# Kernel tuning notes

Measured on AMD Instinct MI355X. Metric: run time of the kernel, lower is better.

The kernel has to match this reference:

```python
import jax, jax.numpy as jnp
import numpy as np

N_USERS = 100000
N_LOCAS = 50000
N = N_USERS + N_LOCAS
D = 128   # embedding_dynamic_size
K = 128   # kg entity dim
S = 128   # static dim
NK = 50000  # kg rows
E = 2048  # number of events
LN_EPS = 1e-5
NORM_EPS = 1e-12


def setup_inputs() -> dict:
    key = jax.random.key(0)
    ks = jax.random.split(key, 24)
    f = jnp.float32
    rin = D + K + 1
    s_rnn = 1.0 / np.sqrt(D)
    s_pred = 1.0 / np.sqrt(2 * S + 2 * D + K)
    inp = {
        'embedding': jax.random.normal(ks[0], (N, D), f),
        'static': jax.random.normal(ks[1], (N, S), f),
        'kg': jax.random.normal(ks[2], (NK, K), f),
        'W_ih_u': jax.random.normal(ks[3], (D, rin), f) * s_rnn,
        'b_ih_u': jax.random.normal(ks[4], (D,), f) * s_rnn,
        'W_hh_u': jax.random.normal(ks[5], (D, D), f) * s_rnn,
        'b_hh_u': jax.random.normal(ks[6], (D,), f) * s_rnn,
        'W_ih_l': jax.random.normal(ks[7], (D, rin), f) * s_rnn,
        'b_ih_l': jax.random.normal(ks[8], (D,), f) * s_rnn,
        'W_hh_l': jax.random.normal(ks[9], (D, D), f) * s_rnn,
        'b_hh_l': jax.random.normal(ks[10], (D,), f) * s_rnn,
        'w_proj': jax.random.normal(ks[11], (D,), f),   # NormalLinear(1, D) weight, std=1/sqrt(1)=1
        'b_proj': jax.random.normal(ks[12], (D,), f),
        'ln_g': jnp.ones((D + K,), f),
        'ln_b': jnp.zeros((D + K,), f),
        'W_pred': jax.random.normal(ks[13], (S + D, 2 * S + 2 * D + K), f) * s_pred,
        'b_pred': jnp.zeros((S + D,), f),
        'delta_u': jax.random.uniform(ks[14], (E,), f),
        'delta_l': jax.random.uniform(ks[15], (E,), f),
        'idx_user': jax.random.randint(ks[16], (E,), 0, N_USERS, jnp.int32),
        'idx_loca': jax.random.randint(ks[17], (E,), 0, N_LOCAS, jnp.int32),
        'idx_prev': jax.random.randint(ks[18], (E,), 0, N_LOCAS, jnp.int32),
        'idx_know': jax.random.randint(ks[19], (E,), 0, NK, jnp.int32),
        'num_users': N_USERS,
    }
    return inp


def reference(embedding, static, kg, W_ih_u, b_ih_u, W_hh_u, b_hh_u,
              W_ih_l, b_ih_l, W_hh_l, b_hh_l, w_proj, b_proj, ln_g, ln_b,
              W_pred, b_pred, delta_u, delta_l,
              idx_user, idx_loca, idx_prev, idx_know, num_users):
    sg = jax.lax.stop_gradient

    def l2n(x):  # F.normalize along the feature dim (row vector)
        return x / jnp.maximum(jnp.linalg.norm(x), NORM_EPS)

    # event index preprocessing (matches idx_loca + num_users etc.)
    xs = (idx_user, idx_loca + num_users, idx_prev + num_users, idx_know,
          delta_u, delta_l)

    def step(carry, ev):
        emb, loss = carry
        iu, il, ip, ik, du, dl = ev
        u = emb[iu]        # [D]
        l = emb[il]        # [D]
        p = emb[ip]        # [D]
        kgr = kg[ik]       # [K]
        # projection: u * (1 + Linear(1->D)(delta_u))
        proj = u * (1.0 + w_proj * du + b_proj)
        # layer_norm over concat([emb_prev, kg_row]) of size D+K
        x = jnp.concatenate([p, kgr])
        mu = x.mean()
        var = jnp.mean((x - mu) ** 2)
        ln = (x - mu) / jnp.sqrt(var + LN_EPS) * ln_g + ln_b
        meta = jnp.concatenate([proj, ln, static[ip], static[iu]])  # [2S+2D+K]
        pred = W_pred @ meta + b_pred                               # [S+D]
        tgt = jnp.concatenate([l, static[il]])
        loss_pred = jnp.mean((pred - sg(tgt)) ** 2)
        # RNNCell updates (tanh), then L2-normalize
        x_u = jnp.concatenate([l, kgr, du[None]])
        new_u = l2n(jnp.tanh(W_ih_u @ x_u + b_ih_u + W_hh_u @ u + b_hh_u))
        x_l = jnp.concatenate([u, kgr, dl[None]])
        new_l = l2n(jnp.tanh(W_ih_l @ x_l + b_ih_l + W_hh_l @ l + b_hh_l))
        loss = loss + loss_pred \
                    + jnp.mean((new_u - sg(u)) ** 2) \
                    + jnp.mean((new_l - sg(l)) ** 2)
        emb = emb.at[iu].set(new_u).at[il].set(new_l)
        return (emb, loss), None

    (emb, loss), _ = jax.lax.scan(
        step, (embedding, jnp.asarray(0.0, embedding.dtype)), xs)
    return emb, loss
```

## Files before the change

### kernel.cpp

```cpp
#include <hip/hip_runtime.h>

#define DEVINL static __device__ __forceinline__

typedef float f32x4 __attribute__((ext_vector_type(4)));

constexpr int NUSER = 100000;
constexpr int D     = 128;
constexpr int METAN = 640;
constexpr int NT    = 256;
constexpr int CH    = 4;
constexpr int KP4   = 160;
constexpr int KR4   = 96;
constexpr int NCPY  = 2048;

struct Params {
  const float *emb_in, *stat, *kg;
  const float *Wihu, *bihu, *Whhu, *bhhu;
  const float *Wihl, *bihl, *Whhl, *bhhl;
  const float *wproj, *bproj, *lng, *lnb, *Wpred, *bpred;
  const float *deltau, *deltal;
  const int *idxu, *idxl, *idxp, *idxk;
  float *emb;
  float *loss_slot;
  float *WpredT;
  float *WrnnT;
  float *brnn;
  float *wcol;
  float *loss_ev;
  int *cnt_u, *cnt_w, *cnt_t;
  int *flag_u, *flag_l;
  int E, N, NLOC, NWORK;
};

DEVINL float loadx(const float* p) {
  return __hip_atomic_load(p, __ATOMIC_RELAXED, __HIP_MEMORY_SCOPE_AGENT);
}
DEVINL void storex(float* p, float v) {
  __hip_atomic_store(p, v, __ATOMIC_RELAXED, __HIP_MEMORY_SCOPE_AGENT);
}
DEVINL int loadcnt(const int* p) {
  return __hip_atomic_load(p, __ATOMIC_RELAXED, __HIP_MEMORY_SCOPE_AGENT);
}
DEVINL void sigadd(int* pp) {
  __hip_atomic_fetch_add(pp, 1, __ATOMIC_RELAXED, __HIP_MEMORY_SCOPE_AGENT);
}
DEVINL float dot4(float4 a, float4 b) { return a.x*b.x + a.y*b.y + a.z*b.z + a.w*b.w; }

DEVINL float4 block_sum4(float4 v, float4* s4) {
  #pragma unroll
  for (int o = 32; o; o >>= 1) {
    v.x += __shfl_xor(v.x, o, 64); v.y += __shfl_xor(v.y, o, 64);
    v.z += __shfl_xor(v.z, o, 64); v.w += __shfl_xor(v.w, o, 64);
  }
  if ((threadIdx.x & 63) == 0) s4[threadIdx.x >> 6] = v;
  __syncthreads();
  float4 r;
  r.x = s4[0].x + s4[1].x + s4[2].x + s4[3].x;
  r.y = s4[0].y + s4[1].y + s4[2].y + s4[3].y;
  r.z = s4[0].z + s4[1].z + s4[2].z + s4[3].z;
  r.w = s4[0].w + s4[1].w + s4[2].w + s4[3].w;
  __syncthreads();
  return r;
}

DEVINL void half_sum4(float4 v, float4* s4, float4* lo, float4* hi) {
  #pragma unroll
  for (int o = 32; o; o >>= 1) {
    v.x += __shfl_xor(v.x, o, 64); v.y += __shfl_xor(v.y, o, 64);
    v.z += __shfl_xor(v.z, o, 64); v.w += __shfl_xor(v.w, o, 64);
  }
  if ((threadIdx.x & 63) == 0) s4[threadIdx.x >> 6] = v;
  __syncthreads();
  lo->x = s4[0].x + s4[1].x; lo->y = s4[0].y + s4[1].y;
  lo->z = s4[0].z + s4[1].z; lo->w = s4[0].w + s4[1].w;
  hi->x = s4[2].x + s4[3].x; hi->y = s4[2].y + s4[3].y;
  hi->z = s4[2].z + s4[3].z; hi->w = s4[2].w + s4[3].w;
  __syncthreads();
}

__global__ void k_init(Params p) {
  int tid = blockIdx.x * NT + threadIdx.x;
  int stride = gridDim.x * NT;
  for (int e = tid; e < p.E; e += stride) {
    p.flag_u[p.idxu[e]] = 1;
    p.flag_l[p.idxl[e]] = 1;
  }
  for (int idx = tid; idx < 256 * KP4; idx += stride) {
    int j = idx / KP4, k4 = idx - j * KP4;
    float4 v = *(const float4*)(p.Wpred + (size_t)j * METAN + k4 * 4);
    ((float4*)p.WpredT)[k4 * 256 + j] = v;
  }
  for (int idx = tid; idx < 256 * KR4; idx += stride) {
    int j = idx / KR4, k4 = idx - j * KR4;
    int i = j & 127;
    const float* Wih = (j < 128) ? p.Wihu : p.Wihl;
    const float* Whh = (j < 128) ? p.Whhu : p.Whhl;
    float4 v; float* vp = (float*)&v;
    #pragma unroll
    for (int e = 0; e < 4; ++e) {
      int k = k4 * 4 + e;
      vp[e] = (k < 256) ? Wih[(size_t)i * 257 + k] : Whh[(size_t)i * 128 + (k - 256)];
    }
    ((float4*)p.WrnnT)[k4 * 256 + j] = v;
  }
  for (int j = tid; j < 256; j += stride) {
    int i = j & 127;
    p.brnn[j] = (j < 128) ? p.bihu[i] + p.bhhu[i] : p.bihl[i] + p.bhhl[i];
    p.wcol[j] = (j < 128) ? p.Wihu[(size_t)i * 257 + 256] : p.Wihl[(size_t)i * 257 + 256];
  }
}

__global__ __launch_bounds__(NT) void k_copy(Params p) {
  size_t gid = (size_t)blockIdx.x * NT + threadIdx.x;
  size_t gs  = (size_t)gridDim.x * NT;
  size_t n4  = (size_t)p.N * 32;
  const f32x4* src = (const f32x4*)p.emb_in;
  f32x4* dst = (f32x4*)p.emb;
  size_t g = gid;
  for (; g + 3 * gs < n4; g += 4 * gs) {
    size_t g0 = g, g1 = g + gs, g2 = g + 2 * gs, g3 = g + 3 * gs;
    int r0 = (int)(g0 >> 5), r1 = (int)(g1 >> 5), r2 = (int)(g2 >> 5), r3 = (int)(g3 >> 5);
    int f0 = (r0 < NUSER) ? p.flag_u[r0] : p.flag_l[r0 - NUSER];
    int f1 = (r1 < NUSER) ? p.flag_u[r1] : p.flag_l[r1 - NUSER];
    int f2 = (r2 < NUSER) ? p.flag_u[r2] : p.flag_l[r2 - NUSER];
    int f3 = (r3 < NUSER) ? p.flag_u[r3] : p.flag_l[r3 - NUSER];
    f32x4 v0 = src[g0], v1 = src[g1], v2 = src[g2], v3 = src[g3];
    if (!f0) dst[g0] = v0;
    if (!f1) dst[g1] = v1;
    if (!f2) dst[g2] = v2;
    if (!f3) dst[g3] = v3;
  }
  for (; g < n4; g += gs) {
    int r = (int)(g >> 5);
    int f = (r < NUSER) ? p.flag_u[r] : p.flag_l[r - NUSER];
    f32x4 v = src[g];
    if (!f) dst[g] = v;
  }
}

__global__ __launch_bounds__(NT, 2) void k_events(Params p) {
  __shared__ __align__(16) float s_meta[CH][METAN];
  __shared__ __align__(16) float s_u[CH][D], s_l[CH][D], s_p[CH][D], s_kg[CH][D], s_sil[CH][D];
  __shared__ float4 s_r4[4];
  __shared__ unsigned long long s_redu[4][CH];
  __shared__ int s_ev[8][CH];
  __shared__ float s_dd[2][CH];

  const int tid = threadIdx.x, w = tid >> 6, lane = tid & 63;

  const int base = blockIdx.x * CH;
  const int nev  = min(CH, p.E - base);
  if (nev <= 0) return;

  int iu_[CH], il_[CH], ip_[CH], ik_[CH];
  float du_[CH], dl_[CH];
  #pragma unroll
  for (int e = 0; e < CH; ++e) {
    int t = base + e; bool v = e < nev;
    iu_[e] = v ? p.idxu[t] : -1;
    il_[e] = v ? p.idxl[t] : -1;
    ip_[e] = v ? p.idxp[t] : -1;
    ik_[e] = v ? p.idxk[t] : 0;
    du_[e] = v ? p.deltau[t] : 0.f;
    dl_[e] = v ? p.deltal[t] : 0.f;
  }

  unsigned long long pk[CH] = {0ull,0ull,0ull,0ull};
  for (int s = tid; s < base; s += NT) {
    int ius = p.idxu[s], ils = p.idxl[s], ips = p.idxp[s];
    #pragma unroll
    for (int e = 0; e < CH; ++e) {
      unsigned long long a  = (ius == iu_[e]);
      unsigned long long wl = (ils == il_[e]);
      unsigned long long b  = (unsigned long long)((ils == il_[e]) + (ips == il_[e]));
      unsigned long long c  = (ils == ip_[e]);
      pk[e] += a | (wl << 16) | (b << 32) | (c << 48);
    }
  }
  #pragma unroll
  for (int o = 32; o; o >>= 1) {
    #pragma unroll
    for (int e = 0; e < CH; ++e) pk[e] += __shfl_xor(pk[e], o, 64);
  }
  if (lane == 0) {
    #pragma unroll
    for (int e = 0; e < CH; ++e) s_redu[w][e] = pk[e];
  }
  __syncthreads();
  #pragma unroll
  for (int e = 0; e < CH; ++e)
    pk[e] = s_redu[0][e] + s_redu[1][e] + s_redu[2][e] + s_redu[3][e];
  __syncthreads();

  int A_[CH], WL_[CH], B_[CH], C_[CH];
  #pragma unroll
  for (int e = 0; e < CH; ++e) {
    int a  = (int)(pk[e] & 0xffff),        wl = (int)((pk[e] >> 16) & 0xffff);
    int b  = (int)((pk[e] >> 32) & 0xffff), c = (int)((pk[e] >> 48) & 0xffff);
    #pragma unroll
    for (int s2 = 0; s2 < CH; ++s2) if (s2 < e) {
      a  += (iu_[s2] == iu_[e]);
      wl += (il_[s2] == il_[e]);
      b  += (il_[s2] == il_[e]) + (ip_[s2] == il_[e]);
      c  += (il_[s2] == ip_[e]);
    }
    A_[e] = a; WL_[e] = wl; B_[e] = b; C_[e] = c;
  }
  bool internal = false;
  #pragma unroll
  for (int t2 = 1; t2 < CH; ++t2) if (t2 < nev) {
    #pragma unroll
    for (int s2 = 0; s2 < t2; ++s2)
      internal |= (iu_[s2] == iu_[t2]) | (il_[s2] == il_[t2]) |
                  (il_[s2] == ip_[t2]) | (ip_[s2] == il_[t2]);
  }

  if (tid == 0) {
    #pragma unroll
    for (int e = 0; e < CH; ++e) {
      s_ev[0][e] = iu_[e]; s_ev[1][e] = il_[e]; s_ev[2][e] = ip_[e];
      s_ev[3][e] = A_[e];  s_ev[4][e] = WL_[e]; s_ev[5][e] = B_[e];
      s_ev[6][e] = C_[e];  s_ev[7][e] = ik_[e];
      s_dd[0][e] = du_[e]; s_dd[1][e] = dl_[e];
    }
  }
  __syncthreads();

  auto PRELOAD = [&](int b0, int b1) {
    int e = w;
    if (e >= b0 && e < b1) {
      int iu = s_ev[0][e], ilr = s_ev[1][e] + NUSER, ipr = s_ev[2][e] + NUSER;
      int A = s_ev[3][e], WL = s_ev[4][e], Ck = s_ev[6][e], ik = s_ev[7][e];
      int h2 = lane >> 5, li = (lane & 31) * 4;
      if (h2 == 0) {
        *(float4*)&s_kg[e][li]         = *(const float4*)(p.kg   + (size_t)ik  * D + li);
        *(float4*)&s_meta[e][512 + li] = *(const float4*)(p.stat + (size_t)iu  * D + li);
      } else {
        *(float4*)&s_meta[e][384 + li] = *(const float4*)(p.stat + (size_t)ipr * D + li);
        *(float4*)&s_sil[e][li]        = *(const float4*)(p.stat + (size_t)ilr * D + li);
      }
      int i0 = lane * 2;
      if (!A) {
        *(float2*)&s_u[e][i0] = *(const float2*)(p.emb_in + (size_t)iu * D + i0);
      }
      if (!WL) {
        *(float2*)&s_l[e][i0] = *(const float2*)(p.emb_in + (size_t)ilr * D + i0);
      }
      if (!Ck) {
        *(float2*)&s_p[e][i0] = *(const float2*)(p.emb_in + (size_t)ipr * D + i0);
      }
    }
  };

  auto SPIN = [&](int b0, int b1) {
    if (w == 0) {
      int e = b0 + lane;
      bool act = lane < (b1 - b0);
      int iu = 0, il = 0, ip = 0, A = 0, Bc = 0, Cc = 0;
      if (act) {
        iu = s_ev[0][e]; il = s_ev[1][e]; ip = s_ev[2][e];
        A = s_ev[3][e]; Bc = s_ev[5][e]; Cc = s_ev[6][e];
      }
      int guard = 0;
      while (true) {
        int x = loadcnt(&p.cnt_u[iu]);
        int y = loadcnt(&p.cnt_t[il]);
        int z = loadcnt(&p.cnt_w[ip]);
        bool ok = (!act) | ((x >= A) & (y >= Bc) & (z >= Cc));
        if (__all(ok)) break;
        if (++guard > (1 << 22)) break;
        __builtin_amdgcn_s_sleep(1);
      }
    }
    __syncthreads();
  };

  auto POSTLOAD = [&](int b0, int b1) {
    int e = w;
    if (e >= b0 && e < b1) {
      int iu = s_ev[0][e], ilr = s_ev[1][e] + NUSER, ipr = s_ev[2][e] + NUSER;
      int A = s_ev[3][e], WL = s_ev[4][e], Ck = s_ev[6][e];
      int i0 = lane * 2;
      if (A) {
        s_u[e][i0]   = loadx(p.emb + (size_t)iu * D + i0);
        s_u[e][i0+1] = loadx(p.emb + (size_t)iu * D + i0 + 1);
      }
      if (WL) {
        s_l[e][i0]   = loadx(p.emb + (size_t)ilr * D + i0);
        s_l[e][i0+1] = loadx(p.emb + (size_t)ilr * D + i0 + 1);
      }
      if (Ck) {
        s_p[e][i0]   = loadx(p.emb + (size_t)ipr * D + i0);
        s_p[e][i0+1] = loadx(p.emb + (size_t)ipr * D + i0 + 1);
      }
    }
  };

  auto PROCESS = [&](int b0, int b1) {
    __syncthreads();

    const bool uc = (tid < 128);
    const float4* xo0 = (const float4*)(uc ? s_l[0] : s_u[0]);
    const float4* xo1 = (const float4*)(uc ? s_l[1] : s_u[1]);
    const float4* xo2 = (const float4*)(uc ? s_l[2] : s_u[2]);
    const float4* xo3 = (const float4*)(uc ? s_l[3] : s_u[3]);
    const float4* xk0 = (const float4*)s_kg[0];
    const float4* xk1 = (const float4*)s_kg[1];
    const float4* xk2 = (const float4*)s_kg[2];
    const float4* xk3 = (const float4*)s_kg[3];
    const float4* xs0 = (const float4*)(uc ? s_u[0] : s_l[0]);
    const float4* xs1 = (const float4*)(uc ? s_u[1] : s_l[1]);
    const float4* xs2 = (const float4*)(uc ? s_u[2] : s_l[2]);
    const float4* xs3 = (const float4*)(uc ? s_u[3] : s_l[3]);
    float ra0 = 0.f, ra1 = 0.f, ra2 = 0.f, ra3 = 0.f;
    const float4* wr = (const float4*)p.WrnnT + tid;
    #pragma unroll 8
    for (int k4 = 0; k4 < 32; ++k4) {
      float4 wv = wr[k4 * 256];
      ra0 += dot4(wv, xo0[k4]); ra1 += dot4(wv, xo1[k4]);
      ra2 += dot4(wv, xo2[k4]); ra3 += dot4(wv, xo3[k4]);
    }
    #pragma unroll 8
    for (int k4 = 32; k4 < 64; ++k4) {
      float4 wv = wr[k4 * 256];
      ra0 += dot4(wv, xk0[k4-32]); ra1 += dot4(wv, xk1[k4-32]);
      ra2 += dot4(wv, xk2[k4-32]); ra3 += dot4(wv, xk3[k4-32]);
    }
    #pragma unroll 8
    for (int k4 = 64; k4 < 96; ++k4) {
      float4 wv = wr[k4 * 256];
      ra0 += dot4(wv, xs0[k4-64]); ra1 += dot4(wv, xs1[k4-64]);
      ra2 += dot4(wv, xs2[k4-64]); ra3 += dot4(wv, xs3[k4-64]);
    }
    float brn = p.brnn[tid], wcv = p.wcol[tid];
    float d0 = uc ? s_dd[0][0] : s_dd[1][0];
    float d1 = uc ? s_dd[0][1] : s_dd[1][1];
    float d2 = uc ? s_dd[0][2] : s_dd[1][2];
    float d3 = uc ? s_dd[0][3] : s_dd[1][3];
    float h0 = tanhf(ra0 + brn + wcv * d0), h1 = tanhf(ra1 + brn + wcv * d1);
    float h2v = tanhf(ra2 + brn + wcv * d2), h3 = tanhf(ra3 + brn + wcv * d3);

    float4 SU, SL;
    half_sum4(make_float4(h0*h0, h1*h1, h2v*h2v, h3*h3), s_r4, &SU, &SL);
    float s0 = uc ? SU.x : SL.x, s1 = uc ? SU.y : SL.y;
    float s2 = uc ? SU.z : SL.z, s3 = uc ? SU.w : SL.w;
    float n0 = h0 / fmaxf(sqrtf(s0), 1e-12f), n1 = h1 / fmaxf(sqrtf(s1), 1e-12f);
    float n2 = h2v / fmaxf(sqrtf(s2), 1e-12f), n3 = h3 / fmaxf(sqrtf(s3), 1e-12f);

    float nv[CH] = {n0, n1, n2, n3};
    #pragma unroll
    for (int e = 0; e < CH; ++e) if (e >= b0 && e < b1) {
      if (tid < 128) storex(p.emb + (size_t)s_ev[0][e] * D + tid, nv[e]);
      else           storex(p.emb + ((size_t)s_ev[1][e] + NUSER) * D + (tid - 128), nv[e]);
    }
    __syncthreads();

    if (tid >= b0 && tid < b1) {
      __builtin_amdgcn_fence(__ATOMIC_RELEASE, "agent");
      sigadd(&p.cnt_u[s_ev[0][tid]]);
      sigadd(&p.cnt_t[s_ev[1][tid]]);
      sigadd(&p.cnt_w[s_ev[1][tid]]);
      sigadd(&p.cnt_t[s_ev[2][tid]]);
    }

    {
      int e = w;
      if (e >= b0 && e < b1) {
        float du = s_dd[0][e];
        float4 xv = (lane < 32) ? *(const float4*)&s_p[e][lane * 4]
                                : *(const float4*)&s_kg[e][(lane - 32) * 4];
        float sm = xv.x + xv.y + xv.z + xv.w;
        #pragma unroll
        for (int o = 32; o; o >>= 1) sm += __shfl_xor(sm, o, 64);
        float mu = sm * (1.f / 256.f);
        float4 d = make_float4(xv.x - mu, xv.y - mu, xv.z - mu, xv.w - mu);
        float vs = d.x*d.x + d.y*d.y + d.z*d.z + d.w*d.w;
        #pragma unroll
        for (int o = 32; o; o >>= 1) vs += __shfl_xor(vs, o, 64);
        float rstd = rsqrtf(vs * (1.f / 256.f) + 1e-5f);
        int idx = lane * 4;
        float4 g  = *(const float4*)&p.lng[idx];
        float4 bb = *(const float4*)&p.lnb[idx];
        *(float4*)&s_meta[e][128 + idx] = make_float4(
          d.x*rstd*g.x + bb.x, d.y*rstd*g.y + bb.y,
          d.z*rstd*g.z + bb.z, d.w*rstd*g.w + bb.w);

        int i0 = lane * 2;
        #pragma unroll
        for (int j = 0; j < 2; ++j) {
          int i = i0 + j;
          s_meta[e][i] = s_u[e][i] * (1.f + p.wproj[i] * du + p.bproj[i]);
        }
      }
    }
    __syncthreads();

    const float4* m40 = (const float4*)&s_meta[0][0];
    const float4* m41 = (const float4*)&s_meta[1][0];
    const float4* m42 = (const float4*)&s_meta[2][0];
    const float4* m43 = (const float4*)&s_meta[3][0];
    float pa0 = 0.f, pa1 = 0.f, pa2 = 0.f, pa3 = 0.f;
    const float4* wp = (const float4*)p.WpredT + tid;
    #pragma unroll 8
    for (int k4 = 0; k4 < KP4; ++k4) {
      float4 wv = wp[k4 * 256];
      pa0 += dot4(wv, m40[k4]); pa1 += dot4(wv, m41[k4]);
      pa2 += dot4(wv, m42[k4]); pa3 += dot4(wv, m43[k4]);
    }
    float bp = p.bpred[tid];
    float4 ep2;
    {
      float tg0 = uc ? s_l[0][tid] : s_sil[0][tid - 128];
      float tg1 = uc ? s_l[1][tid] : s_sil[1][tid - 128];
      float tg2 = uc ? s_l[2][tid] : s_sil[2][tid - 128];
      float tg3 = uc ? s_l[3][tid] : s_sil[3][tid - 128];
      float e0 = pa0 + bp - tg0, e1 = pa1 + bp - tg1;
      float e2 = pa2 + bp - tg2, e3 = pa3 + bp - tg3;
      ep2 = make_float4(e0*e0, e1*e1, e2*e2, e3*e3);
    }
    float4 LP = block_sum4(ep2, s_r4);

    float o0 = uc ? s_u[0][tid] : s_l[0][tid - 128];
    float o1 = uc ? s_u[1][tid] : s_l[1][tid - 128];
    float o2 = uc ? s_u[2][tid] : s_l[2][tid - 128];
    float o3 = uc ? s_u[3][tid] : s_l[3][tid - 128];
    float q0 = n0 - o0, q1 = n1 - o1, q2 = n2 - o2, q3 = n3 - o3;
    float4 LE = block_sum4(make_float4(q0*q0, q1*q1, q2*q2, q3*q3), s_r4);

    if (tid >= b0 && tid < b1) {
      float lp = (tid == 0) ? LP.x : (tid == 1) ? LP.y : (tid == 2) ? LP.z : LP.w;
      float le = (tid == 0) ? LE.x : (tid == 1) ? LE.y : (tid == 2) ? LE.z : LE.w;
      p.loss_ev[base + tid] = lp * (1.f / 256.f) + le * (1.f / 128.f);
    }
  };

  if (!internal) {
    PRELOAD(0, nev);
    SPIN(0, nev);
    POSTLOAD(0, nev);
    PROCESS(0, nev);
  } else {
    for (int e = 0; e < nev; ++e) {
      PRELOAD(e, e + 1);
      SPIN(e, e + 1);
      POSTLOAD(e, e + 1);
      PROCESS(e, e + 1);
    }
  }
}

__global__ void k_fin(Params p) {
  __shared__ float4 s_r4[4];
  float v = 0.f;
  for (int i = threadIdx.x; i < p.E; i += NT) v += p.loss_ev[i];
  float4 r = block_sum4(make_float4(v, 0.f, 0.f, 0.f), s_r4);
  if (threadIdx.x == 0) p.loss_slot[0] = r.x;
}

extern "C" void kernel_launch(void* const* d_in, const int* in_sizes, int n_in,
                              void* d_out, int out_size, void* d_ws, size_t ws_size,
                              hipStream_t stream) {
  Params p;
  p.emb_in = (const float*)d_in[0];
  p.stat   = (const float*)d_in[1];
  p.kg     = (const float*)d_in[2];
  p.Wihu = (const float*)d_in[3];   p.bihu = (const float*)d_in[4];
  p.Whhu = (const float*)d_in[5];   p.bhhu = (const float*)d_in[6];
  p.Wihl = (const float*)d_in[7];   p.bihl = (const float*)d_in[8];
  p.Whhl = (const float*)d_in[9];   p.bhhl = (const float*)d_in[10];
  p.wproj = (const float*)d_in[11]; p.bproj = (const float*)d_in[12];
  p.lng  = (const float*)d_in[13];  p.lnb  = (const float*)d_in[14];
  p.Wpred = (const float*)d_in[15]; p.bpred = (const float*)d_in[16];
  p.deltau = (const float*)d_in[17];
  p.deltal = (const float*)d_in[18];
  p.idxu = (const int*)d_in[19];
  p.idxl = (const int*)d_in[20];
  p.idxp = (const int*)d_in[21];
  p.idxk = (const int*)d_in[22];

  p.E    = in_sizes[17];
  p.N    = in_sizes[0] / D;
  p.NLOC = p.N - NUSER;
  p.NWORK = (p.E + CH - 1) / CH;

  p.emb       = (float*)d_out;
  p.loss_slot = (float*)d_out + (size_t)p.N * D;

  char* ws = (char*)d_ws;
  size_t off = 0;
  auto take = [&](size_t bytes) {
    void* r = ws + off;
    off += (bytes + 255) & ~(size_t)255;
    return r;
  };
  p.WpredT  = (float*)take((size_t)KP4 * 256 * 16);
  p.WrnnT   = (float*)take((size_t)KR4 * 256 * 16);
  p.brnn    = (float*)take(256 * 4);
  p.wcol    = (float*)take(256 * 4);
  p.loss_ev = (float*)take((size_t)p.E * 4);
  size_t z0 = off;
  p.cnt_u   = (int*)take((size_t)NUSER * 4);
  p.cnt_w   = (int*)take((size_t)p.NLOC * 4);
  p.cnt_t   = (int*)take((size_t)p.NLOC * 4);
  p.flag_u  = (int*)take((size_t)NUSER * 4);
  p.flag_l  = (int*)take((size_t)p.NLOC * 4);
  size_t zbytes = off - z0;

  hipMemsetAsync(ws + z0, 0, zbytes, stream);
  hipLaunchKernelGGL(k_init,   dim3(512),    dim3(NT), 0, stream, p);
  hipLaunchKernelGGL(k_copy,   dim3(NCPY),   dim3(NT), 0, stream, p);
  hipLaunchKernelGGL(k_events, dim3(p.NWORK),dim3(NT), 0, stream, p);
  hipLaunchKernelGGL(k_fin,    dim3(1),      dim3(NT), 0, stream, p);
}
```

Measured before the change: 173.8 us.

## Fuse copy into event kernel and split RNN chain from prediction-loss blocks

```diff
diff --git a/kernel.cpp b/kernel.cpp
--- a/kernel.cpp
+++ b/kernel.cpp
@@ -11,7 +11,8 @@
 constexpr int CH    = 4;
 constexpr int KP4   = 160;
 constexpr int KR4   = 96;
-constexpr int NCPY  = 2048;
+constexpr int NCPY  = 1024;
+constexpr int STW   = 640;
 
 struct Params {
   const float *emb_in, *stat, *kg;
@@ -27,8 +28,10 @@
   float *brnn;
   float *wcol;
   float *loss_ev;
+  float *stash;
   int *cnt_u, *cnt_w, *cnt_t;
   int *flag_u, *flag_l;
+  int *done;
   int E, N, NLOC, NWORK;
 };
 
@@ -40,6 +43,9 @@
 }
 DEVINL int loadcnt(const int* p) {
   return __hip_atomic_load(p, __ATOMIC_RELAXED, __HIP_MEMORY_SCOPE_AGENT);
+}
+DEVINL void storei(int* p, int v) {
+  __hip_atomic_store(p, v, __ATOMIC_RELAXED, __HIP_MEMORY_SCOPE_AGENT);
 }
 DEVINL void sigadd(int* pp) {
   __hip_atomic_fetch_add(pp, 1, __ATOMIC_RELAXED, __HIP_MEMORY_SCOPE_AGENT);
@@ -110,35 +116,7 @@
   }
 }
 
-__global__ __launch_bounds__(NT) void k_copy(Params p) {
-  size_t gid = (size_t)blockIdx.x * NT + threadIdx.x;
-  size_t gs  = (size_t)gridDim.x * NT;
-  size_t n4  = (size_t)p.N * 32;
-  const f32x4* src = (const f32x4*)p.emb_in;
-  f32x4* dst = (f32x4*)p.emb;
-  size_t g = gid;
-  for (; g + 3 * gs < n4; g += 4 * gs) {
-    size_t g0 = g, g1 = g + gs, g2 = g + 2 * gs, g3 = g + 3 * gs;
-    int r0 = (int)(g0 >> 5), r1 = (int)(g1 >> 5), r2 = (int)(g2 >> 5), r3 = (int)(g3 >> 5);
-    int f0 = (r0 < NUSER) ? p.flag_u[r0] : p.flag_l[r0 - NUSER];
-    int f1 = (r1 < NUSER) ? p.flag_u[r1] : p.flag_l[r1 - NUSER];
-    int f2 = (r2 < NUSER) ? p.flag_u[r2] : p.flag_l[r2 - NUSER];
-    int f3 = (r3 < NUSER) ? p.flag_u[r3] : p.flag_l[r3 - NUSER];
-    f32x4 v0 = src[g0], v1 = src[g1], v2 = src[g2], v3 = src[g3];
-    if (!f0) dst[g0] = v0;
-    if (!f1) dst[g1] = v1;
-    if (!f2) dst[g2] = v2;
-    if (!f3) dst[g3] = v3;
-  }
-  for (; g < n4; g += gs) {
-    int r = (int)(g >> 5);
-    int f = (r < NUSER) ? p.flag_u[r] : p.flag_l[r - NUSER];
-    f32x4 v = src[g];
-    if (!f) dst[g] = v;
-  }
-}
-
-__global__ __launch_bounds__(NT, 2) void k_events(Params p) {
+__global__ __launch_bounds__(NT, 2) void k_main(Params p) {
   __shared__ __align__(16) float s_meta[CH][METAN];
   __shared__ __align__(16) float s_u[CH][D], s_l[CH][D], s_p[CH][D], s_kg[CH][D], s_sil[CH][D];
   __shared__ float4 s_r4[4];
@@ -147,13 +125,44 @@
   __shared__ float s_dd[2][CH];
 
   const int tid = threadIdx.x, w = tid >> 6, lane = tid & 63;
-
-  const int base = blockIdx.x * CH;
-  const int nev  = min(CH, p.E - base);
+  const int bid = blockIdx.x;
+
+  if (bid >= p.NWORK && bid < p.NWORK + NCPY) {
+    size_t gid = (size_t)(bid - p.NWORK) * NT + tid;
+    size_t gs  = (size_t)NCPY * NT;
+    size_t n4  = (size_t)p.N * 32;
+    const f32x4* src = (const f32x4*)p.emb_in;
+    f32x4* dst = (f32x4*)p.emb;
+    size_t g = gid;
+    for (; g + 3 * gs < n4; g += 4 * gs) {
+      size_t g0 = g, g1 = g + gs, g2 = g + 2 * gs, g3 = g + 3 * gs;
+      int r0 = (int)(g0 >> 5), r1 = (int)(g1 >> 5), r2 = (int)(g2 >> 5), r3 = (int)(g3 >> 5);
+      int f0 = (r0 < NUSER) ? p.flag_u[r0] : p.flag_l[r0 - NUSER];
+      int f1 = (r1 < NUSER) ? p.flag_u[r1] : p.flag_l[r1 - NUSER];
+      int f2 = (r2 < NUSER) ? p.flag_u[r2] : p.flag_l[r2 - NUSER];
+      int f3 = (r3 < NUSER) ? p.flag_u[r3] : p.flag_l[r3 - NUSER];
+      f32x4 v0 = src[g0], v1 = src[g1], v2 = src[g2], v3 = src[g3];
+      if (!f0) dst[g0] = v0;
+      if (!f1) dst[g1] = v1;
+      if (!f2) dst[g2] = v2;
+      if (!f3) dst[g3] = v3;
+    }
+    for (; g < n4; g += gs) {
+      int r = (int)(g >> 5);
+      int f = (r < NUSER) ? p.flag_u[r] : p.flag_l[r - NUSER];
+      f32x4 v = src[g];
+      if (!f) dst[g] = v;
+    }
+    return;
+  }
+
+  const bool is_chain = (bid < p.NWORK);
+  const int c = is_chain ? bid : bid - p.NWORK - NCPY;
+  const int base = c * CH;
+  const int nev = min(CH, p.E - base);
   if (nev <= 0) return;
 
   int iu_[CH], il_[CH], ip_[CH], ik_[CH];
-  float du_[CH], dl_[CH];
   #pragma unroll
   for (int e = 0; e < CH; ++e) {
     int t = base + e; bool v = e < nev;
@@ -161,76 +170,258 @@
     il_[e] = v ? p.idxl[t] : -1;
     ip_[e] = v ? p.idxp[t] : -1;
     ik_[e] = v ? p.idxk[t] : 0;
-    du_[e] = v ? p.deltau[t] : 0.f;
-    dl_[e] = v ? p.deltal[t] : 0.f;
-  }
-
-  unsigned long long pk[CH] = {0ull,0ull,0ull,0ull};
-  for (int s = tid; s < base; s += NT) {
-    int ius = p.idxu[s], ils = p.idxl[s], ips = p.idxp[s];
+  }
+
+  if (is_chain) {
+    float du_[CH], dl_[CH];
     #pragma unroll
     for (int e = 0; e < CH; ++e) {
-      unsigned long long a  = (ius == iu_[e]);
-      unsigned long long wl = (ils == il_[e]);
-      unsigned long long b  = (unsigned long long)((ils == il_[e]) + (ips == il_[e]));
-      unsigned long long c  = (ils == ip_[e]);
-      pk[e] += a | (wl << 16) | (b << 32) | (c << 48);
-    }
-  }
-  #pragma unroll
-  for (int o = 32; o; o >>= 1) {
+      int t = base + e; bool v = e < nev;
+      du_[e] = v ? p.deltau[t] : 0.f;
+      dl_[e] = v ? p.deltal[t] : 0.f;
+    }
+
+    unsigned long long pk[CH] = {0ull,0ull,0ull,0ull};
+    for (int s = tid; s < base; s += NT) {
+      int ius = p.idxu[s], ils = p.idxl[s], ips = p.idxp[s];
+      #pragma unroll
+      for (int e = 0; e < CH; ++e) {
+        unsigned long long a  = (ius == iu_[e]);
+        unsigned long long wl = (ils == il_[e]);
+        unsigned long long b  = (unsigned long long)((ils == il_[e]) + (ips == il_[e]));
+        unsigned long long cc = (ils == ip_[e]);
+        pk[e] += a | (wl << 16) | (b << 32) | (cc << 48);
+      }
+    }
     #pragma unroll
-    for (int e = 0; e < CH; ++e) pk[e] += __shfl_xor(pk[e], o, 64);
-  }
-  if (lane == 0) {
+    for (int o = 32; o; o >>= 1) {
+      #pragma unroll
+      for (int e = 0; e < CH; ++e) pk[e] += __shfl_xor(pk[e], o, 64);
+    }
+    if (lane == 0) {
+      #pragma unroll
+      for (int e = 0; e < CH; ++e) s_redu[w][e] = pk[e];
+    }
+    __syncthreads();
     #pragma unroll
-    for (int e = 0; e < CH; ++e) s_redu[w][e] = pk[e];
-  }
-  __syncthreads();
-  #pragma unroll
-  for (int e = 0; e < CH; ++e)
-    pk[e] = s_redu[0][e] + s_redu[1][e] + s_redu[2][e] + s_redu[3][e];
-  __syncthreads();
-
-  int A_[CH], WL_[CH], B_[CH], C_[CH];
-  #pragma unroll
-  for (int e = 0; e < CH; ++e) {
-    int a  = (int)(pk[e] & 0xffff),        wl = (int)((pk[e] >> 16) & 0xffff);
-    int b  = (int)((pk[e] >> 32) & 0xffff), c = (int)((pk[e] >> 48) & 0xffff);
-    #pragma unroll
-    for (int s2 = 0; s2 < CH; ++s2) if (s2 < e) {
-      a  += (iu_[s2] == iu_[e]);
-      wl += (il_[s2] == il_[e]);
-      b  += (il_[s2] == il_[e]) + (ip_[s2] == il_[e]);
-      c  += (il_[s2] == ip_[e]);
-    }
-    A_[e] = a; WL_[e] = wl; B_[e] = b; C_[e] = c;
-  }
-  bool internal = false;
-  #pragma unroll
-  for (int t2 = 1; t2 < CH; ++t2) if (t2 < nev) {
-    #pragma unroll
-    for (int s2 = 0; s2 < t2; ++s2)
-      internal |= (iu_[s2] == iu_[t2]) | (il_[s2] == il_[t2]) |
-                  (il_[s2] == ip_[t2]) | (ip_[s2] == il_[t2]);
-  }
-
-  if (tid == 0) {
+    for (int e = 0; e < CH; ++e)
+      pk[e] = s_redu[0][e] + s_redu[1][e] + s_redu[2][e] + s_redu[3][e];
+    __syncthreads();
+
+    int A_[CH], WL_[CH], B_[CH], C_[CH];
     #pragma unroll
     for (int e = 0; e < CH; ++e) {
-      s_ev[0][e] = iu_[e]; s_ev[1][e] = il_[e]; s_ev[2][e] = ip_[e];
-      s_ev[3][e] = A_[e];  s_ev[4][e] = WL_[e]; s_ev[5][e] = B_[e];
-      s_ev[6][e] = C_[e];  s_ev[7][e] = ik_[e];
-      s_dd[0][e] = du_[e]; s_dd[1][e] = dl_[e];
-    }
-  }
-  __syncthreads();
-
-  auto PRELOAD = [&](int b0, int b1) {
-    int e = w;
-    if (e >= b0 && e < b1) {
-      int iu = s_ev[0][e], ilr = s_ev[1][e] + NUSER, ipr = s_ev[2][e] + NUSER;
-      int A = s_ev[3][e], WL = s_ev[4][e], Ck = s_ev[6][e], ik = s_ev[7][e];
+      int a  = (int)(pk[e] & 0xffff),        wl = (int)((pk[e] >> 16) & 0xffff);
+      int b  = (int)((pk[e] >> 32) & 0xffff), cc = (int)((pk[e] >> 48) & 0xffff);
+      #pragma unroll
+      for (int s2 = 0; s2 < CH; ++s2) if (s2 < e) {
+        a  += (iu_[s2] == iu_[e]);
+        wl += (il_[s2] == il_[e]);
+        b  += (il_[s2] == il_[e]) + (ip_[s2] == il_[e]);
+        cc += (il_[s2] == ip_[e]);
+      }
+      A_[e] = a; WL_[e] = wl; B_[e] = b; C_[e] = cc;
+    }
+    bool internal = false;
+    #pragma unroll
+    for (int t2 = 1; t2 < CH; ++t2) if (t2 < nev) {
+      #pragma unroll
+      for (int s2 = 0; s2 < t2; ++s2)
+        internal |= (iu_[s2] == iu_[t2]) | (il_[s2] == il_[t2]) |
+                    (il_[s2] == ip_[t2]) | (ip_[s2] == il_[t2]);
+    }
+
+    if (tid == 0) {
+      #pragma unroll
+      for (int e = 0; e < CH; ++e) {
+        s_ev[0][e] = iu_[e]; s_ev[1][e] = il_[e]; s_ev[2][e] = ip_[e];
+        s_ev[3][e] = A_[e];  s_ev[4][e] = WL_[e]; s_ev[5][e] = B_[e];
+        s_ev[6][e] = C_[e];  s_ev[7][e] = ik_[e];
+        s_dd[0][e] = du_[e]; s_dd[1][e] = dl_[e];
+      }
+    }
+    __syncthreads();
+
+    auto PRELOAD = [&](int b0, int b1) {
+      int e = w;
+      if (e >= b0 && e < b1) {
+        int iu = s_ev[0][e], ilr = s_ev[1][e] + NUSER, ipr = s_ev[2][e] + NUSER;
+        int A = s_ev[3][e], WL = s_ev[4][e], Ck = s_ev[6][e], ik = s_ev[7][e];
+        if (lane < 32) {
+          int li = lane * 4;
+          *(float4*)&s_kg[e][li] = *(const float4*)(p.kg + (size_t)ik * D + li);
+        }
+        int i0 = lane * 2;
+        if (!A)  *(float2*)&s_u[e][i0] = *(const float2*)(p.emb_in + (size_t)iu  * D + i0);
+        if (!WL) *(float2*)&s_l[e][i0] = *(const float2*)(p.emb_in + (size_t)ilr * D + i0);
+        if (!Ck) *(float2*)&s_p[e][i0] = *(const float2*)(p.emb_in + (size_t)ipr * D + i0);
+      }
+    };
+
+    auto SPIN = [&](int b0, int b1) {
+      if (w == 0) {
+        int e = b0 + lane;
+        bool act = lane < (b1 - b0);
+        int iu = 0, il = 0, ip = 0, A = 0, Bc = 0, Cc = 0;
+        if (act) {
+          iu = s_ev[0][e]; il = s_ev[1][e]; ip = s_ev[2][e];
+          A = s_ev[3][e]; Bc = s_ev[5][e]; Cc = s_ev[6][e];
+        }
+        int guard = 0;
+        while (true) {
+          int x = loadcnt(&p.cnt_u[iu]);
+          int y = loadcnt(&p.cnt_t[il]);
+          int z = loadcnt(&p.cnt_w[ip]);
+          bool ok = (!act) | ((x >= A) & (y >= Bc) & (z >= Cc));
+          if (__all(ok)) break;
+          if (++guard > (1 << 22)) break;
+          __builtin_amdgcn_s_sleep(1);
+        }
+      }
+      __syncthreads();
+    };
+
+    auto POSTLOAD = [&](int b0, int b1) {
+      int e = w;
+      if (e >= b0 && e < b1) {
+        int iu = s_ev[0][e], ilr = s_ev[1][e] + NUSER, ipr = s_ev[2][e] + NUSER;
+        int A = s_ev[3][e], WL = s_ev[4][e], Ck = s_ev[6][e];
+        int i0 = lane * 2;
+        if (A) {
+          s_u[e][i0]   = loadx(p.emb + (size_t)iu * D + i0);
+          s_u[e][i0+1] = loadx(p.emb + (size_t)iu * D + i0 + 1);
+        }
+        if (WL) {
+          s_l[e][i0]   = loadx(p.emb + (size_t)ilr * D + i0);
+          s_l[e][i0+1] = loadx(p.emb + (size_t)ilr * D + i0 + 1);
+        }
+        if (Ck) {
+          s_p[e][i0]   = loadx(p.emb + (size_t)ipr * D + i0);
+          s_p[e][i0+1] = loadx(p.emb + (size_t)ipr * D + i0 + 1);
+        }
+      }
+    };
+
+    auto RNNPROC = [&](int b0, int b1) {
+      __syncthreads();
+      const bool uc = (tid < 128);
+      const float4* xo0 = (const float4*)(uc ? s_l[0] : s_u[0]);
+      const float4* xo1 = (const float4*)(uc ? s_l[1] : s_u[1]);
+      const float4* xo2 = (const float4*)(uc ? s_l[2] : s_u[2]);
+      const float4* xo3 = (const float4*)(uc ? s_l[3] : s_u[3]);
+      const float4* xk0 = (const float4*)s_kg[0];
+      const float4* xk1 = (const float4*)s_kg[1];
+      const float4* xk2 = (const float4*)s_kg[2];
+      const float4* xk3 = (const float4*)s_kg[3];
+      const float4* xs0 = (const float4*)(uc ? s_u[0] : s_l[0]);
+      const float4* xs1 = (const float4*)(uc ? s_u[1] : s_l[1]);
+      const float4* xs2 = (const float4*)(uc ? s_u[2] : s_l[2]);
+      const float4* xs3 = (const float4*)(uc ? s_u[3] : s_l[3]);
+      float ra0 = 0.f, ra1 = 0.f, ra2 = 0.f, ra3 = 0.f;
+      const float4* wr = (const float4*)p.WrnnT + tid;
+      #pragma unroll 8
+      for (int k4 = 0; k4 < 32; ++k4) {
+        float4 wv = wr[k4 * 256];
+        ra0 += dot4(wv, xo0[k4]); ra1 += dot4(wv, xo1[k4]);
+        ra2 += dot4(wv, xo2[k4]); ra3 += dot4(wv, xo3[k4]);
+      }
+      #pragma unroll 8
+      for (int k4 = 32; k4 < 64; ++k4) {
+        float4 wv = wr[k4 * 256];
+        ra0 += dot4(wv, xk0[k4-32]); ra1 += dot4(wv, xk1[k4-32]);
+        ra2 += dot4(wv, xk2[k4-32]); ra3 += dot4(wv, xk3[k4-32]);
+      }
+      #pragma unroll 8
+      for (int k4 = 64; k4 < 96; ++k4) {
+        float4 wv = wr[k4 * 256];
+        ra0 += dot4(wv, xs0[k4-64]); ra1 += dot4(wv, xs1[k4-64]);
+        ra2 += dot4(wv, xs2[k4-64]); ra3 += dot4(wv, xs3[k4-64]);
+      }
+      float brn = p.brnn[tid], wcv = p.wcol[tid];
+      float d0 = uc ? s_dd[0][0] : s_dd[1][0];
+      float d1 = uc ? s_dd[0][1] : s_dd[1][1];
+      float d2 = uc ? s_dd[0][2] : s_dd[1][2];
+      float d3 = uc ? s_dd[0][3] : s_dd[1][3];
+      float h0 = tanhf(ra0 + brn + wcv * d0), h1 = tanhf(ra1 + brn + wcv * d1);
+      float h2v = tanhf(ra2 + brn + wcv * d2), h3 = tanhf(ra3 + brn + wcv * d3);
+
+      float4 SU, SL;
+      half_sum4(make_float4(h0*h0, h1*h1, h2v*h2v, h3*h3), s_r4, &SU, &SL);
+      float s0 = uc ? SU.x : SL.x, s1 = uc ? SU.y : SL.y;
+      float s2 = uc ? SU.z : SL.z, s3 = uc ? SU.w : SL.w;
+      float n0 = h0 / fmaxf(sqrtf(s0), 1e-12f), n1 = h1 / fmaxf(sqrtf(s1), 1e-12f);
+      float n2 = h2v / fmaxf(sqrtf(s2), 1e-12f), n3 = h3 / fmaxf(sqrtf(s3), 1e-12f);
+
+      float nv[CH] = {n0, n1, n2, n3};
+      #pragma unroll
+      for (int e = 0; e < CH; ++e) if (e >= b0 && e < b1) {
+        if (tid < 128) storex(p.emb + (size_t)s_ev[0][e] * D + tid, nv[e]);
+        else           storex(p.emb + ((size_t)s_ev[1][e] + NUSER) * D + (tid - 128), nv[e]);
+      }
+      __syncthreads();
+
+      if (tid >= b0 && tid < b1) {
+        __builtin_amdgcn_fence(__ATOMIC_RELEASE, "agent");
+        sigadd(&p.cnt_u[s_ev[0][tid]]);
+        sigadd(&p.cnt_t[s_ev[1][tid]]);
+        sigadd(&p.cnt_w[s_ev[1][tid]]);
+        sigadd(&p.cnt_t[s_ev[2][tid]]);
+      }
+
+      #pragma unroll
+      for (int e = 0; e < CH; ++e) if (e >= b0 && e < b1) {
+        float* st = p.stash + (size_t)(base + e) * STW;
+        if (tid < 128) {
+          storex(st + tid,       s_u[e][tid]);
+          storex(st + 256 + tid, s_p[e][tid]);
+          storex(st + 384 + tid, nv[e]);
+        } else {
+          int i = tid - 128;
+          storex(st + 128 + i, s_l[e][i]);
+          storex(st + 512 + i, nv[e]);
+        }
+      }
+    };
+
+    if (!internal) {
+      PRELOAD(0, nev);
+      SPIN(0, nev);
+      POSTLOAD(0, nev);
+      RNNPROC(0, nev);
+    } else {
+      for (int e = 0; e < nev; ++e) {
+        PRELOAD(e, e + 1);
+        SPIN(e, e + 1);
+        POSTLOAD(e, e + 1);
+        RNNPROC(e, e + 1);
+      }
+    }
+    __syncthreads();
+    if (tid == 0) storei(&p.done[c], 1);
+    return;
+  }
+
+  {
+    if (w == 0) {
+      int guard = 0;
+      while (!loadcnt(&p.done[c])) {
+        if (++guard > (1 << 22)) break;
+        __builtin_amdgcn_s_sleep(1);
+      }
+    }
+    __syncthreads();
+
+    if (w < nev) {
+      int e = w;
+      const float* st = p.stash + (size_t)(base + e) * STW;
+      int iu = iu_[e], ilr = il_[e] + NUSER, ipr = ip_[e] + NUSER, ik = ik_[e];
+      int i0 = lane * 2;
+      s_u[e][i0]   = loadx(st + i0);
+      s_u[e][i0+1] = loadx(st + i0 + 1);
+      s_l[e][i0]   = loadx(st + 128 + i0);
+      s_l[e][i0+1] = loadx(st + 128 + i0 + 1);
+      s_p[e][i0]   = loadx(st + 256 + i0);
+      s_p[e][i0+1] = loadx(st + 256 + i0 + 1);
       int h2 = lane >> 5, li = (lane & 31) * 4;
       if (h2 == 0) {
         *(float4*)&s_kg[e][li]         = *(const float4*)(p.kg   + (size_t)ik  * D + li);
@@ -239,162 +430,40 @@
         *(float4*)&s_meta[e][384 + li] = *(const float4*)(p.stat + (size_t)ipr * D + li);
         *(float4*)&s_sil[e][li]        = *(const float4*)(p.stat + (size_t)ilr * D + li);
       }
+    }
+    __syncthreads();
+
+    if (w < nev) {
+      int e = w;
+      float du = p.deltau[base + e];
+      float4 xv = (lane < 32) ? *(const float4*)&s_p[e][lane * 4]
+                              : *(const float4*)&s_kg[e][(lane - 32) * 4];
+      float sm = xv.x + xv.y + xv.z + xv.w;
+      #pragma unroll
+      for (int o = 32; o; o >>= 1) sm += __shfl_xor(sm, o, 64);
+      float mu = sm * (1.f / 256.f);
+      float4 d = make_float4(xv.x - mu, xv.y - mu, xv.z - mu, xv.w - mu);
+      float vs = d.x*d.x + d.y*d.y + d.z*d.z + d.w*d.w;
+      #pragma unroll
+      for (int o = 32; o; o >>= 1) vs += __shfl_xor(vs, o, 64);
+      float rstd = rsqrtf(vs * (1.f / 256.f) + 1e-5f);
+      int idx2 = lane * 4;
+      float4 g  = *(const float4*)&p.lng[idx2];
+      float4 bb = *(const float4*)&p.lnb[idx2];
+      float4 lnv = make_float4(d.x*rstd*g.x + bb.x, d.y*rstd*g.y + bb.y,
+                               d.z*rstd*g.z + bb.z, d.w*rstd*g.w + bb.w);
+      if (lane < 32) *(float4*)&s_meta[e][128 + idx2] = lnv;
+      else           *(float4*)&s_meta[e][128 + idx2] = lnv;
       int i0 = lane * 2;
-      if (!A) {
-        *(float2*)&s_u[e][i0] = *(const float2*)(p.emb_in + (size_t)iu * D + i0);
-      }
-      if (!WL) {
-        *(float2*)&s_l[e][i0] = *(const float2*)(p.emb_in + (size_t)ilr * D + i0);
-      }
-      if (!Ck) {
-        *(float2*)&s_p[e][i0] = *(const float2*)(p.emb_in + (size_t)ipr * D + i0);
-      }
-    }
-  };
-
-  auto SPIN = [&](int b0, int b1) {
-    if (w == 0) {
-      int e = b0 + lane;
-      bool act = lane < (b1 - b0);
-      int iu = 0, il = 0, ip = 0, A = 0, Bc = 0, Cc = 0;
-      if (act) {
-        iu = s_ev[0][e]; il = s_ev[1][e]; ip = s_ev[2][e];
-        A = s_ev[3][e]; Bc = s_ev[5][e]; Cc = s_ev[6][e];
-      }
-      int guard = 0;
-      while (true) {
-        int x = loadcnt(&p.cnt_u[iu]);
-        int y = loadcnt(&p.cnt_t[il]);
-        int z = loadcnt(&p.cnt_w[ip]);
-        bool ok = (!act) | ((x >= A) & (y >= Bc) & (z >= Cc));
-        if (__all(ok)) break;
-        if (++guard > (1 << 22)) break;
-        __builtin_amdgcn_s_sleep(1);
-      }
-    }
-    __syncthreads();
-  };
-
-  auto POSTLOAD = [&](int b0, int b1) {
-    int e = w;
-    if (e >= b0 && e < b1) {
-      int iu = s_ev[0][e], ilr = s_ev[1][e] + NUSER, ipr = s_ev[2][e] + NUSER;
-      int A = s_ev[3][e], WL = s_ev[4][e], Ck = s_ev[6][e];
-      int i0 = lane * 2;
-      if (A) {
-        s_u[e][i0]   = loadx(p.emb + (size_t)iu * D + i0);
-        s_u[e][i0+1] = loadx(p.emb + (size_t)iu * D + i0 + 1);
-      }
-      if (WL) {
-        s_l[e][i0]   = loadx(p.emb + (size_t)ilr * D + i0);
-        s_l[e][i0+1] = loadx(p.emb + (size_t)ilr * D + i0 + 1);
-      }
-      if (Ck) {
-        s_p[e][i0]   = loadx(p.emb + (size_t)ipr * D + i0);
-        s_p[e][i0+1] = loadx(p.emb + (size_t)ipr * D + i0 + 1);
-      }
-    }
-  };
-
-  auto PROCESS = [&](int b0, int b1) {
+      #pragma unroll
+      for (int j = 0; j < 2; ++j) {
+        int i = i0 + j;
+        s_meta[e][i] = s_u[e][i] * (1.f + p.wproj[i] * du + p.bproj[i]);
+      }
+    }
     __syncthreads();
 
     const bool uc = (tid < 128);
-    const float4* xo0 = (const float4*)(uc ? s_l[0] : s_u[0]);
-    const float4* xo1 = (const float4*)(uc ? s_l[1] : s_u[1]);
-    const float4* xo2 = (const float4*)(uc ? s_l[2] : s_u[2]);
-    const float4* xo3 = (const float4*)(uc ? s_l[3] : s_u[3]);
-    const float4* xk0 = (const float4*)s_kg[0];
-    const float4* xk1 = (const float4*)s_kg[1];
-    const float4* xk2 = (const float4*)s_kg[2];
-    const float4* xk3 = (const float4*)s_kg[3];
-    const float4* xs0 = (const float4*)(uc ? s_u[0] : s_l[0]);
-    const float4* xs1 = (const float4*)(uc ? s_u[1] : s_l[1]);
-    const float4* xs2 = (const float4*)(uc ? s_u[2] : s_l[2]);
-    const float4* xs3 = (const float4*)(uc ? s_u[3] : s_l[3]);
-    float ra0 = 0.f, ra1 = 0.f, ra2 = 0.f, ra3 = 0.f;
-    const float4* wr = (const float4*)p.WrnnT + tid;
-    #pragma unroll 8
-    for (int k4 = 0; k4 < 32; ++k4) {
-      float4 wv = wr[k4 * 256];
-      ra0 += dot4(wv, xo0[k4]); ra1 += dot4(wv, xo1[k4]);
-      ra2 += dot4(wv, xo2[k4]); ra3 += dot4(wv, xo3[k4]);
-    }
-    #pragma unroll 8
-    for (int k4 = 32; k4 < 64; ++k4) {
-      float4 wv = wr[k4 * 256];
-      ra0 += dot4(wv, xk0[k4-32]); ra1 += dot4(wv, xk1[k4-32]);
-      ra2 += dot4(wv, xk2[k4-32]); ra3 += dot4(wv, xk3[k4-32]);
-    }
-    #pragma unroll 8
-    for (int k4 = 64; k4 < 96; ++k4) {
-      float4 wv = wr[k4 * 256];
-      ra0 += dot4(wv, xs0[k4-64]); ra1 += dot4(wv, xs1[k4-64]);
-      ra2 += dot4(wv, xs2[k4-64]); ra3 += dot4(wv, xs3[k4-64]);
-    }
-    float brn = p.brnn[tid], wcv = p.wcol[tid];
-    float d0 = uc ? s_dd[0][0] : s_dd[1][0];
-    float d1 = uc ? s_dd[0][1] : s_dd[1][1];
-    float d2 = uc ? s_dd[0][2] : s_dd[1][2];
-    float d3 = uc ? s_dd[0][3] : s_dd[1][3];
-    float h0 = tanhf(ra0 + brn + wcv * d0), h1 = tanhf(ra1 + brn + wcv * d1);
-    float h2v = tanhf(ra2 + brn + wcv * d2), h3 = tanhf(ra3 + brn + wcv * d3);
-
-    float4 SU, SL;
-    half_sum4(make_float4(h0*h0, h1*h1, h2v*h2v, h3*h3), s_r4, &SU, &SL);
-    float s0 = uc ? SU.x : SL.x, s1 = uc ? SU.y : SL.y;
-    float s2 = uc ? SU.z : SL.z, s3 = uc ? SU.w : SL.w;
-    float n0 = h0 / fmaxf(sqrtf(s0), 1e-12f), n1 = h1 / fmaxf(sqrtf(s1), 1e-12f);
-    float n2 = h2v / fmaxf(sqrtf(s2), 1e-12f), n3 = h3 / fmaxf(sqrtf(s3), 1e-12f);
-
-    float nv[CH] = {n0, n1, n2, n3};
-    #pragma unroll
-    for (int e = 0; e < CH; ++e) if (e >= b0 && e < b1) {
-      if (tid < 128) storex(p.emb + (size_t)s_ev[0][e] * D + tid, nv[e]);
-      else           storex(p.emb + ((size_t)s_ev[1][e] + NUSER) * D + (tid - 128), nv[e]);
-    }
-    __syncthreads();
-
-    if (tid >= b0 && tid < b1) {
-      __builtin_amdgcn_fence(__ATOMIC_RELEASE, "agent");
-      sigadd(&p.cnt_u[s_ev[0][tid]]);
-      sigadd(&p.cnt_t[s_ev[1][tid]]);
-      sigadd(&p.cnt_w[s_ev[1][tid]]);
-      sigadd(&p.cnt_t[s_ev[2][tid]]);
-    }
-
-    {
-      int e = w;
-      if (e >= b0 && e < b1) {
-        float du = s_dd[0][e];
-        float4 xv = (lane < 32) ? *(const float4*)&s_p[e][lane * 4]
-                                : *(const float4*)&s_kg[e][(lane - 32) * 4];
-        float sm = xv.x + xv.y + xv.z + xv.w;
-        #pragma unroll
-        for (int o = 32; o; o >>= 1) sm += __shfl_xor(sm, o, 64);
-        float mu = sm * (1.f / 256.f);
-        float4 d = make_float4(xv.x - mu, xv.y - mu, xv.z - mu, xv.w - mu);
-        float vs = d.x*d.x + d.y*d.y + d.z*d.z + d.w*d.w;
-        #pragma unroll
-        for (int o = 32; o; o >>= 1) vs += __shfl_xor(vs, o, 64);
-        float rstd = rsqrtf(vs * (1.f / 256.f) + 1e-5f);
-        int idx = lane * 4;
-        float4 g  = *(const float4*)&p.lng[idx];
-        float4 bb = *(const float4*)&p.lnb[idx];
-        *(float4*)&s_meta[e][128 + idx] = make_float4(
-          d.x*rstd*g.x + bb.x, d.y*rstd*g.y + bb.y,
-          d.z*rstd*g.z + bb.z, d.w*rstd*g.w + bb.w);
-
-        int i0 = lane * 2;
-        #pragma unroll
-        for (int j = 0; j < 2; ++j) {
-          int i = i0 + j;
-          s_meta[e][i] = s_u[e][i] * (1.f + p.wproj[i] * du + p.bproj[i]);
-        }
-      }
-    }
-    __syncthreads();
-
     const float4* m40 = (const float4*)&s_meta[0][0];
     const float4* m41 = (const float4*)&s_meta[1][0];
     const float4* m42 = (const float4*)&s_meta[2][0];
@@ -420,6 +489,13 @@
     }
     float4 LP = block_sum4(ep2, s_r4);
 
+    const float* st0 = p.stash + (size_t)(base + 0) * STW;
+    const float* st1 = p.stash + (size_t)(base + 1) * STW;
+    const float* st2 = p.stash + (size_t)(base + 2) * STW;
+    const float* st3 = p.stash + (size_t)(base + 3) * STW;
+    int noff = uc ? (384 + tid) : (512 + tid - 128);
+    float n0 = loadx(st0 + noff), n1 = loadx(st1 + noff);
+    float n2 = loadx(st2 + noff), n3 = loadx(st3 + noff);
     float o0 = uc ? s_u[0][tid] : s_l[0][tid - 128];
     float o1 = uc ? s_u[1][tid] : s_l[1][tid - 128];
     float o2 = uc ? s_u[2][tid] : s_l[2][tid - 128];
@@ -427,24 +503,10 @@
     float q0 = n0 - o0, q1 = n1 - o1, q2 = n2 - o2, q3 = n3 - o3;
     float4 LE = block_sum4(make_float4(q0*q0, q1*q1, q2*q2, q3*q3), s_r4);
 
-    if (tid >= b0 && tid < b1) {
+    if (tid < nev) {
       float lp = (tid == 0) ? LP.x : (tid == 1) ? LP.y : (tid == 2) ? LP.z : LP.w;
       float le = (tid == 0) ? LE.x : (tid == 1) ? LE.y : (tid == 2) ? LE.z : LE.w;
       p.loss_ev[base + tid] = lp * (1.f / 256.f) + le * (1.f / 128.f);
-    }
-  };
-
-  if (!internal) {
-    PRELOAD(0, nev);
-    SPIN(0, nev);
-    POSTLOAD(0, nev);
-    PROCESS(0, nev);
-  } else {
-    for (int e = 0; e < nev; ++e) {
-      PRELOAD(e, e + 1);
-      SPIN(e, e + 1);
-      POSTLOAD(e, e + 1);
-      PROCESS(e, e + 1);
     }
   }
 }
@@ -498,17 +560,18 @@
   p.brnn    = (float*)take(256 * 4);
   p.wcol    = (float*)take(256 * 4);
   p.loss_ev = (float*)take((size_t)p.E * 4);
+  p.stash   = (float*)take((size_t)p.E * STW * 4);
   size_t z0 = off;
   p.cnt_u   = (int*)take((size_t)NUSER * 4);
   p.cnt_w   = (int*)take((size_t)p.NLOC * 4);
   p.cnt_t   = (int*)take((size_t)p.NLOC * 4);
   p.flag_u  = (int*)take((size_t)NUSER * 4);
   p.flag_l  = (int*)take((size_t)p.NLOC * 4);
+  p.done    = (int*)take((size_t)p.NWORK * 4);
   size_t zbytes = off - z0;
 
   hipMemsetAsync(ws + z0, 0, zbytes, stream);
-  hipLaunchKernelGGL(k_init,   dim3(512),    dim3(NT), 0, stream, p);
-  hipLaunchKernelGGL(k_copy,   dim3(NCPY),   dim3(NT), 0, stream, p);
-  hipLaunchKernelGGL(k_events, dim3(p.NWORK),dim3(NT), 0, stream, p);
-  hipLaunchKernelGGL(k_fin,    dim3(1),      dim3(NT), 0, stream, p);
-}
+  hipLaunchKernelGGL(k_init, dim3(512), dim3(NT), 0, stream, p);
+  hipLaunchKernelGGL(k_main, dim3(p.NWORK * 2 + NCPY), dim3(NT), 0, stream, p);
+  hipLaunchKernelGGL(k_fin,  dim3(1),   dim3(NT), 0, stream, p);
+}
```

Result: faster. 144.1 us (-17.0%).
